# Kernel tuning notes

Hardware: AMD Instinct MI355X
Metric: run time of the kernel (lower is better)

Reference implementation:

```python
import jax, jax.numpy as jnp
import numpy as np

HEADS = 8

def setup_inputs() -> dict:
    key = jax.random.key(0)
    ks = jax.random.split(key, 11)
    B, S, E = 4, 2048, 512
    sc = 1.0 / np.sqrt(E)
    return {
        "inputs": jax.random.normal(ks[0], (B, S, E), jnp.float32),
        "entangle": jax.random.uniform(ks[1], (S,), jnp.float32),
        "Wq": jax.random.normal(ks[2], (E, E), jnp.float32) * sc,
        "bq": jax.random.normal(ks[3], (E,), jnp.float32) * 0.01,
        "Wk": jax.random.normal(ks[4], (E, E), jnp.float32) * sc,
        "bk": jax.random.normal(ks[5], (E,), jnp.float32) * 0.01,
        "Wv": jax.random.normal(ks[6], (E, E), jnp.float32) * sc,
        "bv": jax.random.normal(ks[7], (E,), jnp.float32) * 0.01,
        "Wo": jax.random.normal(ks[8], (E, E), jnp.float32) * sc,
        "bo": jax.random.normal(ks[9], (E,), jnp.float32) * 0.01,
    }

def reference(inputs, entangle, Wq, bq, Wk, bk, Wv, bv, Wo, bo):
    B, S, E = inputs.shape
    H = HEADS
    D = E // H
    # torch nn.Linear: y = x @ W.T + b
    Q = (inputs @ Wq.T + bq).reshape(B, S, H, D)
    K = (inputs @ Wk.T + bk).reshape(B, S, H, D)
    V = (inputs @ Wv.T + bv).reshape(B, S, H, D)
    scores = jnp.einsum('bqhd,bkhd->bhqk', Q, K) / jnp.sqrt(jnp.float32(D))
    # entangle broadcast as (1,1,S,1): per-query-position scaling before softmax
    scores = scores * entangle[None, None, :, None]
    attn = jax.nn.softmax(scores, axis=-1)
    out = jnp.einsum('bhqk,bkhd->bqhd', attn, V).reshape(B, S, E)
    return out @ Wo.T + bo
```

## Files before the change

kernel.cpp:

```cpp
#include <hip/hip_runtime.h>
#include <hip/hip_bf16.h>

#define BB 4
#define SS 2048
#define EE 512
#define HH 8
#define DD 64

typedef __attribute__((ext_vector_type(8))) short bf16x8;
typedef __attribute__((ext_vector_type(4))) float f32x4;
typedef __attribute__((ext_vector_type(4))) unsigned int u32x4;

__device__ __forceinline__ unsigned short f2bf(float f) {
    __hip_bfloat16 h = __float2bfloat16(f);
    return *reinterpret_cast<unsigned short*>(&h);
}

__device__ __forceinline__ unsigned int cvtpk(float lo, float hi) {
    unsigned int r;
    asm("v_cvt_pk_bf16_f32 %0, %1, %2" : "=v"(r) : "v"(lo), "v"(hi));
    return r;
}

__device__ __forceinline__ float ex2(float x) {
    float r;
    asm("v_exp_f32 %0, %1" : "=v"(r) : "v"(x));
    return r;
}

__device__ __forceinline__ void pl32(unsigned int& a, unsigned int& b) {
    asm("v_permlane32_swap_b32 %0, %1" : "+v"(a), "+v"(b));
}
__device__ __forceinline__ void pl16(unsigned int& a, unsigned int& b) {
    asm("v_permlane16_swap_b32 %0, %1" : "+v"(a), "+v"(b));
}

__device__ __forceinline__ void gll16(const unsigned short* g, unsigned short* l) {
    __builtin_amdgcn_global_load_lds(
        (const __attribute__((address_space(1))) unsigned int*)g,
        (__attribute__((address_space(3))) unsigned int*)l,
        16, 0, 0);
}

__global__ __launch_bounds__(256)
void cast_all(const float* __restrict__ x,
              const float* __restrict__ wq, const float* __restrict__ wk,
              const float* __restrict__ wv, const float* __restrict__ wo,
              unsigned short* __restrict__ xb,
              unsigned short* __restrict__ wqb, unsigned short* __restrict__ wkb,
              unsigned short* __restrict__ wvb, unsigned short* __restrict__ wob)
{
    const int bid = blockIdx.x;
    const float* src; unsigned short* dst; int lb;
    if (bid < 4096)      { src = x;  dst = xb;  lb = bid; }
    else {
        const int t = (bid - 4096) >> 8;
        lb = (bid - 4096) & 255;
        switch (t) {
            case 0:  src = wq; dst = wqb; break;
            case 1:  src = wk; dst = wkb; break;
            case 2:  src = wv; dst = wvb; break;
            default: src = wo; dst = wob; break;
        }
    }
    const int i = lb * 256 + threadIdx.x;
    const float4 v = reinterpret_cast<const float4*>(src)[i];
    ushort4 o;
    o.x = f2bf(v.x); o.y = f2bf(v.y); o.z = f2bf(v.z); o.w = f2bf(v.w);
    reinterpret_cast<ushort4*>(dst)[i] = o;
}

template<typename OutT, bool TRANSPOSE_V, int TM>
__global__ __launch_bounds__(256)
void gemm_mfma_nt(const unsigned short* __restrict__ A,
                  const unsigned short* __restrict__ W0, const float* __restrict__ b0, OutT* __restrict__ C0,
                  const unsigned short* __restrict__ W1, const float* __restrict__ b1, OutT* __restrict__ C1,
                  const unsigned short* __restrict__ W2, const float* __restrict__ b2, OutT* __restrict__ C2,
                  const float* __restrict__ rowscale,
                  int M, int N, int K)
{
    const unsigned short* W = (blockIdx.z == 0) ? W0 : (blockIdx.z == 1) ? W1 : W2;
    const float* bias       = (blockIdx.z == 0) ? b0 : (blockIdx.z == 1) ? b1 : b2;
    OutT* C                 = (blockIdx.z == 0) ? C0 : (blockIdx.z == 1) ? C1 : C2;

    constexpr int MT  = TM / 32;
    constexpr int STG = 3 * TM * 32;
    __shared__ unsigned short lds[STG + 3 * 128 * 32];
    unsigned short* As = lds;
    unsigned short* Bs = lds + STG;

    const int tid  = threadIdx.x;
    const int wave = tid >> 6, lane = tid & 63;
    const int quad = lane >> 4, r16 = lane & 15;
    const int m0 = blockIdx.x * TM, n0 = blockIdx.y * 128;
    const int wm0 = (wave >> 1) * (TM / 2), wn0 = (wave & 1) * 64;

    f32x4 acc[MT][4];
    const f32x4 zero = {0.f, 0.f, 0.f, 0.f};
    #pragma unroll
    for (int i = 0; i < MT; ++i)
        #pragma unroll
        for (int j = 0; j < 4; ++j) acc[i][j] = zero;

    const int swz = (r16 >> 1) & 3;

    auto stage = [&](int bi, int k0) {
        #pragma unroll
        for (int j = 0; j < TM / 64; ++j) {
            const int cb = wave * 64 + j * 256;
            const int c  = cb + lane;
            const int row = c >> 2, cc = (c & 3) ^ ((row >> 1) & 3);
            gll16(&A[(size_t)(m0 + row) * K + k0 + cc * 8], &As[bi * TM * 32 + cb * 8]);
        }
        #pragma unroll
        for (int j = 0; j < 2; ++j) {
            const int cb = wave * 64 + j * 256;
            const int c  = cb + lane;
            const int row = c >> 2, cc = (c & 3) ^ ((row >> 1) & 3);
            gll16(&W[(size_t)(n0 + row) * K + k0 + cc * 8], &Bs[bi * 128 * 32 + cb * 8]);
        }
    };

    stage(0, 0);
    stage(1, 32);

    const int NI = K / 32;
    for (int i = 0; i < NI; ++i) {
        const int cur = i % 3;
        if (i + 1 < NI) {
            if constexpr (TM == 128) asm volatile("s_waitcnt vmcnt(4)" ::: "memory");
            else                     asm volatile("s_waitcnt vmcnt(3)" ::: "memory");
        } else {
            asm volatile("s_waitcnt vmcnt(0)" ::: "memory");
        }
        __builtin_amdgcn_s_barrier();
        __builtin_amdgcn_sched_barrier(0);
        if (i + 2 < NI) stage((i + 2) % 3, (i + 2) * 32);

        bf16x8 af[MT], bfr[4];
        #pragma unroll
        for (int t = 0; t < MT; ++t)
            af[t]  = *reinterpret_cast<bf16x8*>(&As[cur * TM * 32 + ((wm0 + t * 16 + r16) * 4 + (quad ^ swz)) * 8]);
        #pragma unroll
        for (int t = 0; t < 4; ++t)
            bfr[t] = *reinterpret_cast<bf16x8*>(&Bs[cur * 128 * 32 + ((wn0 + t * 16 + r16) * 4 + (quad ^ swz)) * 8]);
        #pragma unroll
        for (int mt = 0; mt < MT; ++mt)
            #pragma unroll
            for (int nt = 0; nt < 4; ++nt)
                acc[mt][nt] = __builtin_amdgcn_mfma_f32_16x16x32_bf16(
                    af[mt], bfr[nt], acc[mt][nt], 0, 0, 0);
    }

    if (TRANSPOSE_V && blockIdx.z == 2) {
        __syncthreads();
        #pragma unroll
        for (int mt = 0; mt < MT; ++mt) {
            const int s_local = wm0 + mt * 16 + quad * 4;
            #pragma unroll
            for (int nt = 0; nt < 4; ++nt) {
                const int d_local = wn0 + nt * 16 + r16;
                const float bv = bias[n0 + d_local];
                uint2 o;
                o.x = cvtpk(acc[mt][nt][0] + bv, acc[mt][nt][1] + bv);
                o.y = cvtpk(acc[mt][nt][2] + bv, acc[mt][nt][3] + bv);
                *reinterpret_cast<uint2*>(&lds[d_local * 132 + s_local]) = o;
            }
        }
        __syncthreads();
        const int bb = m0 >> 11, s0 = m0 & (SS - 1);
        unsigned short* Vtp = (unsigned short*)C2 + (size_t)bb * EE * SS + s0;
        const int scol = (tid & 15) * 8;
        #pragma unroll
        for (int p = 0; p < 8; ++p) {
            const int row = p * 16 + (tid >> 4);
            const uint2 lo = *reinterpret_cast<const uint2*>(&lds[row * 132 + scol]);
            const uint2 hi = *reinterpret_cast<const uint2*>(&lds[row * 132 + scol + 4]);
            const u32x4 v = {lo.x, lo.y, hi.x, hi.y};
            *reinterpret_cast<u32x4*>(&Vtp[(size_t)(n0 + row) * SS + scol]) = v;
        }
        return;
    }
    if constexpr (sizeof(OutT) == 2) {
        const bool doscale = (rowscale != nullptr) && (blockIdx.z == 0);
        __syncthreads();
        #pragma unroll
        for (int mt = 0; mt < MT; ++mt) {
            float rs[4];
            #pragma unroll
            for (int r = 0; r < 4; ++r) {
                const int row = m0 + wm0 + mt * 16 + quad * 4 + r;
                rs[r] = doscale ? rowscale[row & (SS - 1)] * 0.18033688f : 1.0f;
            }
            #pragma unroll
            for (int nt = 0; nt < 4; ++nt) {
                const int col = wn0 + nt * 16 + r16;
                const float bv = bias[n0 + col];
                #pragma unroll
                for (int r = 0; r < 4; ++r) {
                    const int row = wm0 + mt * 16 + quad * 4 + r;
                    lds[row * 132 + col] = f2bf((acc[mt][nt][r] + bv) * rs[r]);
                }
            }
        }
        __syncthreads();
        const int scol = (tid & 15) * 8;
        #pragma unroll
        for (int p = 0; p < TM / 16; ++p) {
            const int row = p * 16 + (tid >> 4);
            const uint2 lo = *reinterpret_cast<const uint2*>(&lds[row * 132 + scol]);
            const uint2 hi = *reinterpret_cast<const uint2*>(&lds[row * 132 + scol + 4]);
            const u32x4 v = {lo.x, lo.y, hi.x, hi.y};
            *reinterpret_cast<u32x4*>(&((unsigned short*)C)[(size_t)(m0 + row) * N + n0 + scol]) = v;
        }
    } else {
        float* fl = reinterpret_cast<float*>(lds);
        __syncthreads();
        #pragma unroll
        for (int mt = 0; mt < MT; ++mt) {
            #pragma unroll
            for (int nt = 0; nt < 4; ++nt) {
                const int col = wn0 + nt * 16 + r16;
                const float bv = bias[n0 + col];
                #pragma unroll
                for (int r = 0; r < 4; ++r) {
                    const int row = wm0 + mt * 16 + quad * 4 + r;
                    fl[row * 132 + col] = acc[mt][nt][r] + bv;
                }
            }
        }
        __syncthreads();
        const int scol = (tid & 31) * 4;
        #pragma unroll
        for (int p = 0; p < TM / 8; ++p) {
            const int row = p * 8 + (tid >> 5);
            const f32x4 v = *reinterpret_cast<const f32x4*>(&fl[row * 132 + scol]);
            *reinterpret_cast<f32x4*>(&((float*)C)[(size_t)(m0 + row) * N + n0 + scol]) = v;
        }
    }
}

#define QBLK 128
#define KVB  128

__global__ __launch_bounds__(256, 2)
void attn_mfma(const unsigned short* __restrict__ Q,
               const unsigned short* __restrict__ K,
               const unsigned short* __restrict__ Vt,
               unsigned short* __restrict__ O)
{
    __shared__ unsigned short Ks[2][KVB * 64];
    __shared__ unsigned short Vs[2][64 * KVB];

    const int tid  = threadIdx.x;
    const int wave = tid >> 6, lane = tid & 63;
    const int quad = lane >> 4, r16 = lane & 15;
    const int h  = blockIdx.x;
    const int q0 = blockIdx.y * QBLK;
    const int b  = blockIdx.z;
    const size_t base    = (size_t)b * SS * EE + (size_t)h * DD;
    const size_t base_vt = ((size_t)b * HH + h) * DD * SS;

    bf16x8 qf[2][2];
    #pragma unroll
    for (int s = 0; s < 2; ++s) {
        const int qrow = q0 + s * 64 + wave * 16 + r16;
        #pragma unroll
        for (int dh = 0; dh < 2; ++dh)
            qf[s][dh] = *reinterpret_cast<const bf16x8*>(
                &Q[base + (size_t)qrow * EE + dh * 32 + quad * 8]);
    }

    const unsigned short* kp[4];
    const unsigned short* vp[4];
    int cbs[4];
    #pragma unroll
    for (int j = 0; j < 4; ++j) {
        const int cb = wave * 64 + j * 256;
        cbs[j] = cb;
        const int c  = cb + lane;
        const int rowK = c >> 3, ccK = (c & 7) ^ (rowK & 7);
        kp[j] = &K[base + (size_t)rowK * EE + ccK * 8];
        const int rowV = c >> 4, ccV = (c & 15) ^ (rowV & 15);
        vp[j] = &Vt[base_vt + (size_t)rowV * SS + ccV * 8];
    }

    auto stage = [&](int bi, int kt) {
        const size_t ko = (size_t)kt * KVB * EE;
        const int    vo = kt * KVB;
        #pragma unroll
        for (int j = 0; j < 4; ++j) {
            gll16(kp[j] + ko, &Ks[bi][cbs[j] * 8]);
            gll16(vp[j] + vo, &Vs[bi][cbs[j] * 8]);
        }
    };

    float l_lane[2] = {0.f, 0.f};
    f32x4 o_acc[2][4];
    const f32x4 zero = {0.f, 0.f, 0.f, 0.f};
    #pragma unroll
    for (int s = 0; s < 2; ++s)
        #pragma unroll
        for (int dt = 0; dt < 4; ++dt) o_acc[s][dt] = zero;

    const int swz7 = r16 & 7;

    stage(0, 0);

    constexpr int NT = SS / KVB;
    for (int kt = 0; kt < NT; ++kt) {
        const int cur = kt & 1;
        asm volatile("s_waitcnt vmcnt(0)" ::: "memory");
        __builtin_amdgcn_s_barrier();
        __builtin_amdgcn_sched_barrier(0);
        if (kt + 1 < NT) stage(cur ^ 1, kt + 1);

        const unsigned short* Kc = &Ks[cur][0];
        const unsigned short* Vc = &Vs[cur][0];

        f32x4 st[2][8];
        #pragma unroll
        for (int s = 0; s < 2; ++s)
            #pragma unroll
            for (int tn = 0; tn < 8; ++tn) st[s][tn] = zero;
        __builtin_amdgcn_s_setprio(1);
        #pragma unroll
        for (int tn = 0; tn < 8; ++tn) {
            const bf16x8 kf0 = *reinterpret_cast<const bf16x8*>(
                &Kc[((tn * 16 + r16) * 8 + (quad ^ swz7)) * 8]);
            const bf16x8 kf1 = *reinterpret_cast<const bf16x8*>(
                &Kc[((tn * 16 + r16) * 8 + ((quad + 4) ^ swz7)) * 8]);
            #pragma unroll
            for (int s = 0; s < 2; ++s) {
                st[s][tn] = __builtin_amdgcn_mfma_f32_16x16x32_bf16(kf0, qf[s][0], st[s][tn], 0, 0, 0);
                st[s][tn] = __builtin_amdgcn_mfma_f32_16x16x32_bf16(kf1, qf[s][1], st[s][tn], 0, 0, 0);
            }
        }
        __builtin_amdgcn_s_setprio(0);

        bf16x8 pf[2][4];
        #pragma unroll
        for (int s = 0; s < 2; ++s) {
            unsigned int w[8][2];
            #pragma unroll
            for (int tn = 0; tn < 8; ++tn) {
                const float p0 = ex2(st[s][tn][0]);
                const float p1 = ex2(st[s][tn][1]);
                const float p2 = ex2(st[s][tn][2]);
                const float p3 = ex2(st[s][tn][3]);
                l_lane[s] += (p0 + p1) + (p2 + p3);
                w[tn][0] = cvtpk(p0, p1);
                w[tn][1] = cvtpk(p2, p3);
            }
            #pragma unroll
            for (int j = 0; j < 4; ++j) {
                unsigned int a0 = w[2 * j][0], a2 = w[2 * j + 1][0];
                pl32(a0, a2); pl16(a0, a2);
                unsigned int a1 = w[2 * j][1], a3 = w[2 * j + 1][1];
                pl32(a1, a3); pl16(a1, a3);
                const u32x4 u = {a0, a1, a2, a3};
                pf[s][j] = __builtin_bit_cast(bf16x8, u);
            }
        }

        __builtin_amdgcn_s_setprio(1);
        #pragma unroll
        for (int j = 0; j < 4; ++j) {
            #pragma unroll
            for (int dt = 0; dt < 4; ++dt) {
                const bf16x8 vf = *reinterpret_cast<const bf16x8*>(
                    &Vc[((dt * 16 + r16) * 16 + ((4 * j + quad) ^ r16)) * 8]);
                o_acc[0][dt] = __builtin_amdgcn_mfma_f32_16x16x32_bf16(pf[0][j], vf, o_acc[0][dt], 0, 0, 0);
                o_acc[1][dt] = __builtin_amdgcn_mfma_f32_16x16x32_bf16(pf[1][j], vf, o_acc[1][dt], 0, 0, 0);
            }
        }
        __builtin_amdgcn_s_setprio(0);
    }

    float lq[2];
    #pragma unroll
    for (int s = 0; s < 2; ++s) {
        float l = l_lane[s];
        l += __shfl_xor(l, 16, 64);
        l += __shfl_xor(l, 32, 64);
        lq[s] = l;
    }

    unsigned short* ob = &Ks[0][0];
    __syncthreads();
    #pragma unroll
    for (int s = 0; s < 2; ++s) {
        #pragma unroll
        for (int r = 0; r < 4; ++r) {
            const float il = 1.0f / __shfl(lq[s], quad * 4 + r, 64);
            const int ql = s * 64 + wave * 16 + quad * 4 + r;
            #pragma unroll
            for (int dt = 0; dt < 4; ++dt)
                ob[ql * 68 + dt * 16 + r16] = f2bf(o_acc[s][dt][r] * il);
        }
    }
    __syncthreads();
    const int orow = tid >> 3, ocol = (tid & 7) * 8;
    #pragma unroll
    for (int p = 0; p < 4; ++p) {
        const int ql = p * 32 + orow;
        const uint2 lo = *reinterpret_cast<const uint2*>(&ob[ql * 68 + ocol]);
        const uint2 hi = *reinterpret_cast<const uint2*>(&ob[ql * 68 + ocol + 4]);
        const u32x4 v = {lo.x, lo.y, hi.x, hi.y};
        *reinterpret_cast<u32x4*>(&O[base + (size_t)(q0 + ql) * EE + ocol]) = v;
    }
}

extern "C" void kernel_launch(void* const* d_in, const int* in_sizes, int n_in,
                              void* d_out, int out_size, void* d_ws, size_t ws_size,
                              hipStream_t stream) {
    const float* x   = (const float*)d_in[0];
    const float* ent = (const float*)d_in[1];
    const float* Wq  = (const float*)d_in[2];
    const float* bq  = (const float*)d_in[3];
    const float* Wk  = (const float*)d_in[4];
    const float* bk  = (const float*)d_in[5];
    const float* Wv  = (const float*)d_in[6];
    const float* bv  = (const float*)d_in[7];
    const float* Wo  = (const float*)d_in[8];
    const float* bo  = (const float*)d_in[9];
    float* out = (float*)d_out;

    const size_t n_x = (size_t)BB * SS * EE;
    const size_t n_w = (size_t)EE * EE;

    unsigned short* xb  = (unsigned short*)d_ws;
    unsigned short* wqb = xb + n_x;
    unsigned short* wkb = wqb + n_w;
    unsigned short* wvb = wkb + n_w;
    unsigned short* wob = wvb + n_w;
    unsigned short* Qb  = wob + n_w;
    unsigned short* Kb  = Qb + n_x;
    unsigned short* Vtb = Kb + n_x;
    unsigned short* AOb = Vtb + n_x;

    const int M = BB * SS;

    dim3 gc(4096 + 4 * 256, 1, 1);
    cast_all<<<gc, 256, 0, stream>>>(x, Wq, Wk, Wv, Wo, xb, wqb, wkb, wvb, wob);

    dim3 gq(M / 128, EE / 128, 3);
    gemm_mfma_nt<unsigned short, true, 128><<<gq, 256, 0, stream>>>(
        xb, wqb, bq, Qb, wkb, bk, Kb, wvb, bv, Vtb, ent, M, EE, EE);

    dim3 ga(HH, SS / QBLK, BB);
    attn_mfma<<<ga, 256, 0, stream>>>(Qb, Kb, Vtb, AOb);

    dim3 go(M / 64, EE / 128, 1);
    gemm_mfma_nt<float, false, 64><<<go, 256, 0, stream>>>(
        AOb, wob, bo, out, wob, bo, out, wob, bo, out, nullptr, M, EE, EE);
}
```

Before: 158.2 us.

## Fuse fp32-to-bf16 casts into GEMM tile loads, drop separate cast kernel

Removes the standalone cast kernel. The GEMMs now load fp32 activations and weights straight into registers, convert them to bf16 with packed converts, and write them to LDS through a register-staged issue/commit pipeline that replaces the direct global-to-LDS loads. This saves a kernel launch and one round trip of writing and rereading bf16 copies of the input and weights. In exchange, each weight tile is converted again by many blocks, fp32 global reads double the load bytes, and the pipeline now waits on vmcnt(0) every iteration, which weakens load/compute overlap. Occupancy is also hinted with launch bounds of 3.

```diff
diff --git a/kernel.cpp b/kernel.cpp
--- a/kernel.cpp
+++ b/kernel.cpp
@@ -42,48 +42,22 @@
         16, 0, 0);
 }
 
-__global__ __launch_bounds__(256)
-void cast_all(const float* __restrict__ x,
-              const float* __restrict__ wq, const float* __restrict__ wk,
-              const float* __restrict__ wv, const float* __restrict__ wo,
-              unsigned short* __restrict__ xb,
-              unsigned short* __restrict__ wqb, unsigned short* __restrict__ wkb,
-              unsigned short* __restrict__ wvb, unsigned short* __restrict__ wob)
-{
-    const int bid = blockIdx.x;
-    const float* src; unsigned short* dst; int lb;
-    if (bid < 4096)      { src = x;  dst = xb;  lb = bid; }
-    else {
-        const int t = (bid - 4096) >> 8;
-        lb = (bid - 4096) & 255;
-        switch (t) {
-            case 0:  src = wq; dst = wqb; break;
-            case 1:  src = wk; dst = wkb; break;
-            case 2:  src = wv; dst = wvb; break;
-            default: src = wo; dst = wob; break;
-        }
-    }
-    const int i = lb * 256 + threadIdx.x;
-    const float4 v = reinterpret_cast<const float4*>(src)[i];
-    ushort4 o;
-    o.x = f2bf(v.x); o.y = f2bf(v.y); o.z = f2bf(v.z); o.w = f2bf(v.w);
-    reinterpret_cast<ushort4*>(dst)[i] = o;
-}
-
-template<typename OutT, bool TRANSPOSE_V, int TM>
-__global__ __launch_bounds__(256)
-void gemm_mfma_nt(const unsigned short* __restrict__ A,
-                  const unsigned short* __restrict__ W0, const float* __restrict__ b0, OutT* __restrict__ C0,
-                  const unsigned short* __restrict__ W1, const float* __restrict__ b1, OutT* __restrict__ C1,
-                  const unsigned short* __restrict__ W2, const float* __restrict__ b2, OutT* __restrict__ C2,
+template<typename OutT, bool TRANSPOSE_V, int TM, bool AF32>
+__global__ __launch_bounds__(256, 3)
+void gemm_mfma_nt(const unsigned short* __restrict__ Abf,
+                  const float* __restrict__ Af,
+                  const float* __restrict__ W0, const float* __restrict__ b0, OutT* __restrict__ C0,
+                  const float* __restrict__ W1, const float* __restrict__ b1, OutT* __restrict__ C1,
+                  const float* __restrict__ W2, const float* __restrict__ b2, OutT* __restrict__ C2,
                   const float* __restrict__ rowscale,
                   int M, int N, int K)
 {
-    const unsigned short* W = (blockIdx.z == 0) ? W0 : (blockIdx.z == 1) ? W1 : W2;
-    const float* bias       = (blockIdx.z == 0) ? b0 : (blockIdx.z == 1) ? b1 : b2;
-    OutT* C                 = (blockIdx.z == 0) ? C0 : (blockIdx.z == 1) ? C1 : C2;
+    const float* W    = (blockIdx.z == 0) ? W0 : (blockIdx.z == 1) ? W1 : W2;
+    const float* bias = (blockIdx.z == 0) ? b0 : (blockIdx.z == 1) ? b1 : b2;
+    OutT* C           = (blockIdx.z == 0) ? C0 : (blockIdx.z == 1) ? C1 : C2;
 
     constexpr int MT  = TM / 32;
+    constexpr int NA  = TM / 64;
     constexpr int STG = 3 * TM * 32;
     __shared__ unsigned short lds[STG + 3 * 128 * 32];
     unsigned short* As = lds;
@@ -104,38 +78,76 @@
 
     const int swz = (r16 >> 1) & 3;
 
-    auto stage = [&](int bi, int k0) {
-        #pragma unroll
-        for (int j = 0; j < TM / 64; ++j) {
-            const int cb = wave * 64 + j * 256;
-            const int c  = cb + lane;
-            const int row = c >> 2, cc = (c & 3) ^ ((row >> 1) & 3);
-            gll16(&A[(size_t)(m0 + row) * K + k0 + cc * 8], &As[bi * TM * 32 + cb * 8]);
+    int acb[NA > 0 ? NA : 1], arow[NA > 0 ? NA : 1], acc_[NA > 0 ? NA : 1];
+    #pragma unroll
+    for (int j = 0; j < NA; ++j) {
+        const int cb = wave * 64 + j * 256, c = cb + lane;
+        acb[j] = cb; arow[j] = c >> 2; acc_[j] = (c & 3) ^ ((arow[j] >> 1) & 3);
+    }
+    int wcb[2], wrow[2], wcc[2];
+    #pragma unroll
+    for (int j = 0; j < 2; ++j) {
+        const int cb = wave * 64 + j * 256, c = cb + lane;
+        wcb[j] = cb; wrow[j] = c >> 2; wcc[j] = (c & 3) ^ ((wrow[j] >> 1) & 3);
+    }
+
+    f32x4 ra[2 * (NA > 0 ? NA : 1)];
+    f32x4 rw[4];
+
+    auto issue = [&](int bi, int k0) {
+        if constexpr (AF32) {
+            #pragma unroll
+            for (int j = 0; j < NA; ++j) {
+                const float* p = &Af[(size_t)(m0 + arow[j]) * K + k0 + acc_[j] * 8];
+                ra[2 * j]     = *reinterpret_cast<const f32x4*>(p);
+                ra[2 * j + 1] = *reinterpret_cast<const f32x4*>(p + 4);
+            }
+        } else {
+            #pragma unroll
+            for (int j = 0; j < NA; ++j)
+                gll16(&Abf[(size_t)(m0 + arow[j]) * K + k0 + acc_[j] * 8],
+                      &As[bi * TM * 32 + acb[j] * 8]);
         }
         #pragma unroll
         for (int j = 0; j < 2; ++j) {
-            const int cb = wave * 64 + j * 256;
-            const int c  = cb + lane;
-            const int row = c >> 2, cc = (c & 3) ^ ((row >> 1) & 3);
-            gll16(&W[(size_t)(n0 + row) * K + k0 + cc * 8], &Bs[bi * 128 * 32 + cb * 8]);
+            const float* p = &W[(size_t)(n0 + wrow[j]) * K + k0 + wcc[j] * 8];
+            rw[2 * j]     = *reinterpret_cast<const f32x4*>(p);
+            rw[2 * j + 1] = *reinterpret_cast<const f32x4*>(p + 4);
         }
     };
-
-    stage(0, 0);
-    stage(1, 32);
+    auto commit = [&](int bi) {
+        if constexpr (AF32) {
+            #pragma unroll
+            for (int j = 0; j < NA; ++j) {
+                const u32x4 v = {cvtpk(ra[2*j][0], ra[2*j][1]), cvtpk(ra[2*j][2], ra[2*j][3]),
+                                 cvtpk(ra[2*j+1][0], ra[2*j+1][1]), cvtpk(ra[2*j+1][2], ra[2*j+1][3])};
+                *reinterpret_cast<u32x4*>(&As[bi * TM * 32 + (acb[j] + lane) * 8]) = v;
+            }
+        }
+        #pragma unroll
+        for (int j = 0; j < 2; ++j) {
+            const u32x4 v = {cvtpk(rw[2*j][0], rw[2*j][1]), cvtpk(rw[2*j][2], rw[2*j][3]),
+                             cvtpk(rw[2*j+1][0], rw[2*j+1][1]), cvtpk(rw[2*j+1][2], rw[2*j+1][3])};
+            *reinterpret_cast<u32x4*>(&Bs[bi * 128 * 32 + (wcb[j] + lane) * 8]) = v;
+        }
+    };
+
+    issue(0, 0);
+    asm volatile("s_waitcnt vmcnt(0)" ::: "memory");
+    commit(0);
+    issue(1, 32);
 
     const int NI = K / 32;
     for (int i = 0; i < NI; ++i) {
         const int cur = i % 3;
-        if (i + 1 < NI) {
-            if constexpr (TM == 128) asm volatile("s_waitcnt vmcnt(4)" ::: "memory");
-            else                     asm volatile("s_waitcnt vmcnt(3)" ::: "memory");
-        } else {
-            asm volatile("s_waitcnt vmcnt(0)" ::: "memory");
-        }
+        asm volatile("s_waitcnt lgkmcnt(0)" ::: "memory");
         __builtin_amdgcn_s_barrier();
         __builtin_amdgcn_sched_barrier(0);
-        if (i + 2 < NI) stage((i + 2) % 3, (i + 2) * 32);
+        if (i + 1 < NI) {
+            asm volatile("s_waitcnt vmcnt(0)" ::: "memory");
+            commit((i + 1) % 3);
+        }
+        if (i + 2 < NI) issue((i + 2) % 3, (i + 2) * 32);
 
         bf16x8 af[MT], bfr[4];
         #pragma unroll
@@ -441,17 +453,14 @@
 
     const int M = BB * SS;
 
-    dim3 gc(4096 + 4 * 256, 1, 1);
-    cast_all<<<gc, 256, 0, stream>>>(x, Wq, Wk, Wv, Wo, xb, wqb, wkb, wvb, wob);
-
     dim3 gq(M / 128, EE / 128, 3);
-    gemm_mfma_nt<unsigned short, true, 128><<<gq, 256, 0, stream>>>(
-        xb, wqb, bq, Qb, wkb, bk, Kb, wvb, bv, Vtb, ent, M, EE, EE);
+    gemm_mfma_nt<unsigned short, true, 128, true><<<gq, 256, 0, stream>>>(
+        nullptr, x, Wq, bq, Qb, Wk, bk, Kb, Wv, bv, Vtb, ent, M, EE, EE);
 
     dim3 ga(HH, SS / QBLK, BB);
     attn_mfma<<<ga, 256, 0, stream>>>(Qb, Kb, Vtb, AOb);
 
     dim3 go(M / 64, EE / 128, 1);
-    gemm_mfma_nt<float, false, 64><<<go, 256, 0, stream>>>(
-        AOb, wob, bo, out, wob, bo, out, wob, bo, out, nullptr, M, EE, EE);
-}
+    gemm_mfma_nt<float, false, 64, false><<<go, 256, 0, stream>>>(
+        AOb, nullptr, Wo, bo, out, Wo, bo, out, Wo, bo, out, nullptr, M, EE, EE);
+}
```

Result: no change. 156.2 us (-1.3%).
